# Kernel tuning notes

Hardware: AMD Instinct MI355X
Metric: run time of the kernel (lower is better)

## Reference

```python
import jax, jax.numpy as jnp
import numpy as np

N_HEADS = 16
SCALE = 8.0  # sqrt(inner_dim // n_heads) = sqrt(64), scale='inv_sqrt'


def setup_inputs() -> dict:
    key = jax.random.key(0)
    k1, k2, k3, k4 = jax.random.split(key, 4)
    b, n, d_model, inner = 8, 2048, 1024, 1024
    x = jax.random.normal(k1, (b, n, d_model), dtype=jnp.float32)
    Wqkv = jax.random.normal(k2, (3 * inner, d_model), dtype=jnp.float32) * (1.0 / np.sqrt(d_model))
    Wproj = jax.random.normal(k3, (d_model, inner), dtype=jnp.float32) * (1.0 / np.sqrt(inner))
    bproj = jax.random.normal(k4, (d_model,), dtype=jnp.float32) * 0.01
    return {"x": x, "Wqkv": Wqkv, "Wproj": Wproj, "bproj": bproj}


def reference(x, Wqkv, Wproj, bproj):
    b, n, _ = x.shape
    qkv = jnp.einsum('bnm,fm->bnf', x, Wqkv)          # [b, n, 3*inner]
    qkv = qkv.reshape(b, n, N_HEADS, -1)              # [b, n, h, 3*dh] (einops 'b n (h d)')
    dh = qkv.shape[3] // 3
    q, k, v = qkv[..., :dh], qkv[..., dh:2 * dh], qkv[..., 2 * dh:]
    # Faithful to source: q @ k.transpose(-1,-2) on [b,n,h,dh] -> scores over HEADS, [b,n,h,h]
    scores = jnp.einsum('bnhd,bngd->bnhg', q, k) / SCALE
    attn = jax.nn.softmax(scores, axis=-1)            # softmax over last head axis
    out = jnp.einsum('bnhg,bngd->bnhd', attn, v)      # [b, n, h, dh]
    out = out.reshape(b, n, -1)                       # [b, n, inner]
    return jnp.einsum('bni,mi->bnm', out, Wproj) + bproj
```

## Files before the change

kernel.cpp:

```cpp
#include <hip/hip_runtime.h>
#include <stdint.h>

typedef __bf16 bf16_t;
typedef __bf16 bf16x8 __attribute__((ext_vector_type(8)));
typedef float f32x4 __attribute__((ext_vector_type(4)));

__device__ __forceinline__ void gload_lds16(const void* g, void* l) {
  __builtin_amdgcn_global_load_lds(
      (const __attribute__((address_space(1))) uint32_t*)g,
      (__attribute__((address_space(3))) uint32_t*)l, 16, 0, 0);
}

__global__ void cast3_f32_bf16(const float* __restrict__ a, bf16_t* __restrict__ ao, int n4a,
                               const float* __restrict__ b, bf16_t* __restrict__ bo, int n4b,
                               const float* __restrict__ c, bf16_t* __restrict__ co, int n4c) {
  int i = blockIdx.x * blockDim.x + threadIdx.x;
  int stride = gridDim.x * blockDim.x;
  int total = n4a + n4b + n4c;
  for (int idx = i; idx < total; idx += stride) {
    const float* src; bf16_t* dst; int j = idx;
    if (j < n4a) { src = a; dst = ao; }
    else if ((j -= n4a) < n4b) { src = b; dst = bo; }
    else { j -= n4b; src = c; dst = co; }
    float4 v = reinterpret_cast<const float4*>(src)[j];
    union { bf16_t b[4]; uint2 u; } pk;
    pk.b[0] = (bf16_t)v.x; pk.b[1] = (bf16_t)v.y;
    pk.b[2] = (bf16_t)v.z; pk.b[3] = (bf16_t)v.w;
    reinterpret_cast<uint2*>(dst)[j] = pk.u;
  }
}

template <bool BF16_OUT>
__global__ __launch_bounds__(512, 2)
void gemm_pipe(const bf16_t* __restrict__ A, const bf16_t* __restrict__ B,
               void* __restrict__ Cout, const float* __restrict__ bias,
               int N) {
  constexpr int K = 1024, NT = 32;
  __shared__ bf16_t Al[4][256 * 32];
  __shared__ bf16_t Bl[4][256 * 32];

  const int tid = threadIdx.x;
  const int l = tid & 63, w = tid >> 6;
  const int wm = w >> 2, wn = w & 3;

  const int bid = blockIdx.x;
  const int xcd = bid & 7;
  const int idx = bid >> 3;
  const int bx = xcd * 8 + (idx & 7);
  const int by = idx >> 3;
  const int m0 = bx * 256, n0 = by * 256;

  const int ra = tid >> 2;
  const int ca = ((tid & 3) ^ ((tid >> 3) & 3)) * 8;
  const bf16_t* pA0 = A + (size_t)(m0 +   0 + ra) * K + ca;
  const bf16_t* pA1 = A + (size_t)(m0 + 128 + ra) * K + ca;
  const bf16_t* pB0 = B + (size_t)(n0 +   0 + ra) * K + ca;
  const bf16_t* pB1 = B + (size_t)(n0 + 128 + ra) * K + ca;
  const int wb = w * 512;

#define STAGE(t_, s_) do {                          \
    const int kt_ = (t_) * 32;                      \
    gload_lds16(pA0 + kt_, &Al[s_][wb]);            \
    gload_lds16(pA1 + kt_, &Al[s_][4096 + wb]);     \
    gload_lds16(pB0 + kt_, &Bl[s_][wb]);            \
    gload_lds16(pB1 + kt_, &Bl[s_][4096 + wb]);     \
  } while (0)

  const int abase = (wm * 128 + (l & 15)) * 32;
  const int bbase = (wn * 64 + (l & 15)) * 32;
  const int ck = ((l >> 4) ^ ((l >> 1) & 3)) * 8;

  f32x4 acc[8][4] = {};

  STAGE(0, 0);
  STAGE(1, 1);
  STAGE(2, 2);

  int slot = 0;
  for (int t = 0; t < NT; ++t) {
    if (t < NT - 2)       asm volatile("s_waitcnt vmcnt(8)" ::: "memory");
    else if (t == NT - 2) asm volatile("s_waitcnt vmcnt(4)" ::: "memory");
    else                  asm volatile("s_waitcnt vmcnt(0)" ::: "memory");
    __builtin_amdgcn_s_barrier();
    asm volatile("" ::: "memory");
    if (t + 3 < NT) {
      int s3 = (slot + 3) & 3;
      STAGE(t + 3, s3);
    }
    const bf16_t* As = Al[slot];
    const bf16_t* Bs = Bl[slot];
    bf16x8 af[8], bfr[4];
#pragma unroll
    for (int i = 0; i < 8; ++i)
      af[i] = *reinterpret_cast<const bf16x8*>(&As[abase + i * 512 + ck]);
#pragma unroll
    for (int j = 0; j < 4; ++j)
      bfr[j] = *reinterpret_cast<const bf16x8*>(&Bs[bbase + j * 512 + ck]);
    __builtin_amdgcn_s_setprio(1);
#pragma unroll
    for (int i = 0; i < 8; ++i)
#pragma unroll
      for (int j = 0; j < 4; ++j)
        acc[i][j] = __builtin_amdgcn_mfma_f32_16x16x32_bf16(af[i], bfr[j],
                                                            acc[i][j], 0, 0, 0);
    __builtin_amdgcn_s_setprio(0);
    slot = (slot + 1) & 3;
  }
#undef STAGE

  const int r0 = m0 + wm * 128 + (l >> 4) * 4;
  const int c0 = n0 + wn * 64 + (l & 15);
  if (BF16_OUT) {
    bf16_t* C = (bf16_t*)Cout;
#pragma unroll
    for (int i = 0; i < 8; ++i)
#pragma unroll
      for (int j = 0; j < 4; ++j)
#pragma unroll
        for (int r = 0; r < 4; ++r)
          C[(size_t)(r0 + i * 16 + r) * N + (c0 + j * 16)] = (bf16_t)acc[i][j][r];
  } else {
    float* C = (float*)Cout;
#pragma unroll
    for (int i = 0; i < 8; ++i)
#pragma unroll
      for (int j = 0; j < 4; ++j)
#pragma unroll
        for (int r = 0; r < 4; ++r)
          C[(size_t)(r0 + i * 16 + r) * N + (c0 + j * 16)] =
              acc[i][j][r] + bias[c0 + j * 16];
  }
}

__global__ __launch_bounds__(256)
void attn_heads(const bf16_t* __restrict__ qkv, bf16_t* __restrict__ out) {
  __shared__ float s[4][3072];
  const int w = threadIdx.x >> 6, l = threadIdx.x & 63;
  const size_t t = (size_t)blockIdx.x * 4 + w;
  const bf16_t* src = qkv + t * 3072;
#pragma unroll
  for (int i = 0; i < 6; ++i) {
    int f = (i * 64 + l) * 8;
    bf16x8 v = *reinterpret_cast<const bf16x8*>(&src[f]);
#pragma unroll
    for (int jj = 0; jj < 8; ++jj) s[w][f + jj] = (float)v[jj];
  }
  __syncthreads();

  const int h = l >> 2, ss = l & 3;
  float qr[16];
  const float* qb = &s[w][h * 192 + ss * 16];
#pragma unroll
  for (int d = 0; d < 16; ++d) qr[d] = qb[d];

  float sc[16];
#pragma unroll
  for (int g = 0; g < 16; ++g) {
    const float* kk = &s[w][g * 192 + 64 + ss * 16];
    float p = 0.f;
#pragma unroll
    for (int d = 0; d < 16; ++d) p += qr[d] * kk[d];
    p += __shfl_xor(p, 1);
    p += __shfl_xor(p, 2);
    sc[g] = p * 0.125f;
  }
  float m = sc[0];
#pragma unroll
  for (int g = 1; g < 16; ++g) m = fmaxf(m, sc[g]);
  float sum = 0.f;
#pragma unroll
  for (int g = 0; g < 16; ++g) { sc[g] = __expf(sc[g] - m); sum += sc[g]; }
  float inv = 1.f / sum;

  float o[16] = {};
#pragma unroll
  for (int g = 0; g < 16; ++g) {
    float a = sc[g] * inv;
    const float* vv = &s[w][g * 192 + 128 + ss * 16];
#pragma unroll
    for (int d = 0; d < 16; ++d) o[d] += a * vv[d];
  }
  union { bf16_t b[16]; uint4 u[2]; } pk;
#pragma unroll
  for (int d = 0; d < 16; ++d) pk.b[d] = (bf16_t)o[d];
  uint4* dst = reinterpret_cast<uint4*>(out + t * 1024 + h * 64 + ss * 16);
  dst[0] = pk.u[0];
  dst[1] = pk.u[1];
}

extern "C" void kernel_launch(void* const* d_in, const int* in_sizes, int n_in,
                              void* d_out, int out_size, void* d_ws, size_t ws_size,
                              hipStream_t stream) {
  const float* x     = (const float*)d_in[0];
  const float* Wqkv  = (const float*)d_in[1];
  const float* Wproj = (const float*)d_in[2];
  const float* bproj = (const float*)d_in[3];
  float* out = (float*)d_out;

  const int M = 8 * 2048;
  const int DM = 1024;
  const int F = 3072;

  char* ws = (char*)d_ws;
  bf16_t* xb     = (bf16_t*)ws;  ws += (size_t)M * DM * 2;
  bf16_t* wqkvb  = (bf16_t*)ws;  ws += (size_t)F * DM * 2;
  bf16_t* wprojb = (bf16_t*)ws;  ws += (size_t)DM * DM * 2;
  bf16_t* qkvb   = (bf16_t*)ws;  ws += (size_t)M * F * 2;
  bf16_t* attnb  = (bf16_t*)ws;

  cast3_f32_bf16<<<2048, 256, 0, stream>>>(x, xb, M * DM / 4,
                                           Wqkv, wqkvb, F * DM / 4,
                                           Wproj, wprojb, DM * DM / 4);

  gemm_pipe<true><<<(M / 256) * (F / 256), 512, 0, stream>>>(
      xb, wqkvb, (void*)qkvb, nullptr, F);

  attn_heads<<<M / 4, 256, 0, stream>>>(qkvb, attnb);

  gemm_pipe<false><<<(M / 256) * (DM / 256), 512, 0, stream>>>(
      attnb, wprojb, (void*)out, bproj, DM);
}
```

Before: 238.6 us.

## Shrink GEMM tile to 256x128 with 3-stage pipeline for higher occupancy

Replaces the 256x256-tile, 4-stage GEMM with a 256x128 tile, a 3-stage LDS ring and launch bounds targeting 4 blocks per CU. It moves the wait and barrier to the end of each iteration, drops the setprio hints, and changes block-to-tile mapping to a generic nby-based swizzle. The aim is to hide latency through more resident waves and less LDS per block. In exchange, each block has lower arithmetic intensity (more B/A refetch) and a shallower prefetch depth.

```diff
diff --git a/kernel.cpp b/kernel.cpp
--- a/kernel.cpp
+++ b/kernel.cpp
@@ -31,89 +31,79 @@
 }
 
 template <bool BF16_OUT>
-__global__ __launch_bounds__(512, 2)
-void gemm_pipe(const bf16_t* __restrict__ A, const bf16_t* __restrict__ B,
-               void* __restrict__ Cout, const float* __restrict__ bias,
-               int N) {
+__global__ __launch_bounds__(512, 4)
+void gemm_oc(const bf16_t* __restrict__ A, const bf16_t* __restrict__ B,
+             void* __restrict__ Cout, const float* __restrict__ bias,
+             int N, int nby) {
   constexpr int K = 1024, NT = 32;
-  __shared__ bf16_t Al[4][256 * 32];
-  __shared__ bf16_t Bl[4][256 * 32];
+  __shared__ bf16_t Al[3][256 * 32];
+  __shared__ bf16_t Bl[3][128 * 32];
 
   const int tid = threadIdx.x;
   const int l = tid & 63, w = tid >> 6;
-  const int wm = w >> 2, wn = w & 3;
+  const int wm = w >> 1, wn = w & 1;
 
   const int bid = blockIdx.x;
-  const int xcd = bid & 7;
-  const int idx = bid >> 3;
-  const int bx = xcd * 8 + (idx & 7);
-  const int by = idx >> 3;
-  const int m0 = bx * 256, n0 = by * 256;
+  const int xcd = bid & 7, idx = bid >> 3;
+  const int bxsub = idx / nby, by = idx - bxsub * nby;
+  const int bx = xcd * 8 + bxsub;
+  const int m0 = bx * 256, n0 = by * 128;
 
   const int ra = tid >> 2;
   const int ca = ((tid & 3) ^ ((tid >> 3) & 3)) * 8;
-  const bf16_t* pA0 = A + (size_t)(m0 +   0 + ra) * K + ca;
+  const bf16_t* pA0 = A + (size_t)(m0 + ra) * K + ca;
   const bf16_t* pA1 = A + (size_t)(m0 + 128 + ra) * K + ca;
-  const bf16_t* pB0 = B + (size_t)(n0 +   0 + ra) * K + ca;
-  const bf16_t* pB1 = B + (size_t)(n0 + 128 + ra) * K + ca;
-  const int wb = w * 512;
-
-#define STAGE(t_, s_) do {                          \
-    const int kt_ = (t_) * 32;                      \
-    gload_lds16(pA0 + kt_, &Al[s_][wb]);            \
-    gload_lds16(pA1 + kt_, &Al[s_][4096 + wb]);     \
-    gload_lds16(pB0 + kt_, &Bl[s_][wb]);            \
-    gload_lds16(pB1 + kt_, &Bl[s_][4096 + wb]);     \
-  } while (0)
-
-  const int abase = (wm * 128 + (l & 15)) * 32;
+  const bf16_t* pB0 = B + (size_t)(n0 + ra) * K + ca;
+
+#define STAGE(t_, s_) do { const int kt_ = (t_) * 32;  \
+    gload_lds16(pA0 + kt_, &Al[s_][tid * 8]);          \
+    gload_lds16(pA1 + kt_, &Al[s_][4096 + tid * 8]);   \
+    gload_lds16(pB0 + kt_, &Bl[s_][tid * 8]); } while (0)
+
+  const int abase = (wm * 64 + (l & 15)) * 32;
   const int bbase = (wn * 64 + (l & 15)) * 32;
   const int ck = ((l >> 4) ^ ((l >> 1) & 3)) * 8;
 
-  f32x4 acc[8][4] = {};
-
-  STAGE(0, 0);
-  STAGE(1, 1);
-  STAGE(2, 2);
+  f32x4 acc[4][4] = {};
+  bf16x8 af[4], bfr[4];
+
+  STAGE(0, 0); STAGE(1, 1);
+  asm volatile("s_waitcnt vmcnt(3)" ::: "memory");
+  __builtin_amdgcn_s_barrier();
 
   int slot = 0;
   for (int t = 0; t < NT; ++t) {
-    if (t < NT - 2)       asm volatile("s_waitcnt vmcnt(8)" ::: "memory");
-    else if (t == NT - 2) asm volatile("s_waitcnt vmcnt(4)" ::: "memory");
-    else                  asm volatile("s_waitcnt vmcnt(0)" ::: "memory");
-    __builtin_amdgcn_s_barrier();
-    asm volatile("" ::: "memory");
-    if (t + 3 < NT) {
-      int s3 = (slot + 3) & 3;
-      STAGE(t + 3, s3);
-    }
+    int s2 = slot + 2; if (s2 >= 3) s2 -= 3;
+    if (t + 2 < NT) STAGE(t + 2, s2);
     const bf16_t* As = Al[slot];
     const bf16_t* Bs = Bl[slot];
-    bf16x8 af[8], bfr[4];
-#pragma unroll
-    for (int i = 0; i < 8; ++i)
+#pragma unroll
+    for (int i = 0; i < 4; ++i)
       af[i] = *reinterpret_cast<const bf16x8*>(&As[abase + i * 512 + ck]);
 #pragma unroll
     for (int j = 0; j < 4; ++j)
       bfr[j] = *reinterpret_cast<const bf16x8*>(&Bs[bbase + j * 512 + ck]);
-    __builtin_amdgcn_s_setprio(1);
-#pragma unroll
-    for (int i = 0; i < 8; ++i)
+#pragma unroll
+    for (int i = 0; i < 4; ++i)
 #pragma unroll
       for (int j = 0; j < 4; ++j)
         acc[i][j] = __builtin_amdgcn_mfma_f32_16x16x32_bf16(af[i], bfr[j],
                                                             acc[i][j], 0, 0, 0);
-    __builtin_amdgcn_s_setprio(0);
-    slot = (slot + 1) & 3;
+    if (t + 2 < NT) asm volatile("s_waitcnt vmcnt(3)" ::: "memory");
+    else            asm volatile("s_waitcnt vmcnt(0)" ::: "memory");
+    asm volatile("" ::: "memory");
+    __builtin_amdgcn_s_barrier();
+    asm volatile("" ::: "memory");
+    slot = (slot + 1 == 3) ? 0 : slot + 1;
   }
 #undef STAGE
 
-  const int r0 = m0 + wm * 128 + (l >> 4) * 4;
+  const int r0 = m0 + wm * 64 + (l >> 4) * 4;
   const int c0 = n0 + wn * 64 + (l & 15);
   if (BF16_OUT) {
     bf16_t* C = (bf16_t*)Cout;
 #pragma unroll
-    for (int i = 0; i < 8; ++i)
+    for (int i = 0; i < 4; ++i)
 #pragma unroll
       for (int j = 0; j < 4; ++j)
 #pragma unroll
@@ -122,7 +112,7 @@
   } else {
     float* C = (float*)Cout;
 #pragma unroll
-    for (int i = 0; i < 8; ++i)
+    for (int i = 0; i < 4; ++i)
 #pragma unroll
       for (int j = 0; j < 4; ++j)
 #pragma unroll
@@ -212,11 +202,11 @@
                                            Wqkv, wqkvb, F * DM / 4,
                                            Wproj, wprojb, DM * DM / 4);
 
-  gemm_pipe<true><<<(M / 256) * (F / 256), 512, 0, stream>>>(
-      xb, wqkvb, (void*)qkvb, nullptr, F);
+  gemm_oc<true><<<(M / 256) * (F / 128), 512, 0, stream>>>(
+      xb, wqkvb, (void*)qkvb, nullptr, F, F / 128);
 
   attn_heads<<<M / 4, 256, 0, stream>>>(qkvb, attnb);
 
-  gemm_pipe<false><<<(M / 256) * (DM / 256), 512, 0, stream>>>(
-      attnb, wprojb, (void*)out, bproj, DM);
-}
+  gemm_oc<false><<<(M / 256) * (DM / 128), 512, 0, stream>>>(
+      attnb, wprojb, (void*)out, bproj, DM, DM / 128);
+}
```

Result: faster. 219.9 us (-7.8%).
